# Kernel optimization log

Hardware: AMD Instinct MI355X
Metric: run time of the kernel (lower is better)

## Reference

```python
import jax, jax.numpy as jnp
import numpy as np

EPS = 1e-6
NUM_HEADS = 16


def _layernorm(x, g, b):
    m = jnp.mean(x, axis=-1, keepdims=True)
    v = jnp.mean(jnp.square(x - m), axis=-1, keepdims=True)
    return (x - m) * jax.lax.rsqrt(v + EPS) * g + b


def setup_inputs() -> dict:
    key = jax.random.key(0)
    ks = jax.random.split(key, 16)
    B, Lq, Lkv, D = 2, 2048, 4096, 2048
    Hd = D // NUM_HEADS
    s = 0.02
    return {
        "hidden_states": jax.random.normal(ks[0], (B, Lq, D), jnp.float32),
        "cross_attention_states": jax.random.normal(ks[1], (B, Lkv, D), jnp.float32),
        "q_w": jax.random.normal(ks[2], (D, D), jnp.float32) * s,
        "q_b": jnp.zeros((D,), jnp.float32),
        "k_w": jax.random.normal(ks[3], (D, D), jnp.float32) * s,
        "k_b": jnp.zeros((D,), jnp.float32),
        "v_w": jax.random.normal(ks[4], (D, D), jnp.float32) * s,
        "v_b": jnp.zeros((D,), jnp.float32),
        "o_w": jax.random.normal(ks[5], (D, D), jnp.float32) * s,
        "o_b": jnp.zeros((D,), jnp.float32),
        "qn_g": jnp.ones((Hd,), jnp.float32),
        "qn_b": jnp.zeros((Hd,), jnp.float32),
        "kn_g": jnp.ones((Hd,), jnp.float32),
        "kn_b": jnp.zeros((Hd,), jnp.float32),
    }


def reference(hidden_states, cross_attention_states,
              q_w, q_b, k_w, k_b, v_w, v_b, o_w, o_b,
              qn_g, qn_b, kn_g, kn_b):
    B, Lq, D = hidden_states.shape
    H = NUM_HEADS
    Hd = D // H
    scale = Hd ** -0.5

    # torch Linear: y = x @ W^T + b
    q = hidden_states @ q_w.T + q_b                        # [B,Lq,D]
    k = cross_attention_states @ k_w.T + k_b               # [B,Lkv,D]
    v = cross_attention_states @ v_w.T + v_b               # [B,Lkv,D]

    q = q.reshape(B, Lq, H, Hd).transpose(0, 2, 1, 3)      # [B,H,Lq,Hd]
    k = k.reshape(B, -1, H, Hd).transpose(0, 2, 1, 3)      # [B,H,Lkv,Hd]
    v = v.reshape(B, -1, H, Hd).transpose(0, 2, 1, 3)      # [B,H,Lkv,Hd]

    # per-head QK LayerNorm before scores
    q = _layernorm(q, qn_g, qn_b)
    k = _layernorm(k, kn_g, kn_b)

    attn_weights = jnp.einsum('bhqd,bhkd->bhqk', q, k) * scale
    attn_weights = jax.nn.softmax(attn_weights.astype(jnp.float32), axis=-1).astype(q.dtype)
    # dropout p=0.0 (inference) -> identity

    attn_output = jnp.einsum('bhqk,bhkd->bhqd', attn_weights, v)
    attn_output = attn_output.transpose(0, 2, 1, 3).reshape(B, Lq, D)
    attn_output = attn_output @ o_w.T + o_b
    return attn_output, attn_weights
```

## Files before the change

### kernel.cpp

```cpp
#include <hip/hip_runtime.h>
#include <cstdint>
#include <cstddef>

using u16 = unsigned short;
using f32x4 = __attribute__((ext_vector_type(4))) float;
using bf8   = __attribute__((ext_vector_type(8))) short;
using u32x4 = __attribute__((ext_vector_type(4))) unsigned;

#define DEVFN __device__ __forceinline__

constexpr int BB  = 2;
constexpr int LQ  = 2048;
constexpr int LKV = 4096;
constexpr int DD  = 2048;
constexpr int NH  = 16;
constexpr int HDm = 128;
constexpr float ATTN_SCALE = 0.08838834764831845f;
constexpr float LN_EPS = 1e-6f;
constexpr float LOG2E  = 1.4426950408889634f;
constexpr float SHIFT2 = 17.312340490667562f;

DEVFN u16 f2bf(float f) {
  unsigned u = __builtin_bit_cast(unsigned, f);
  u += 0x7fffu + ((u >> 16) & 1u);
  return (u16)(u >> 16);
}
DEVFN float bf2f(u16 h) { return __builtin_bit_cast(float, (unsigned)h << 16); }
DEVFN f32x4 mfma16(bf8 a, bf8 b, f32x4 c) {
  return __builtin_amdgcn_mfma_f32_16x16x32_bf16(a, b, c, 0, 0, 0);
}
DEVFN void gl16(const void* g, void* l) {
  __builtin_amdgcn_global_load_lds(
      (const __attribute__((address_space(1))) void*)g,
      (__attribute__((address_space(3))) void*)l, 16, 0, 0);
}
DEVFN void barrier_hard() {
  __builtin_amdgcn_s_barrier();
  __builtin_amdgcn_sched_barrier(0);
}

__global__ __launch_bounds__(256) void k_cvt(const float4* __restrict__ in,
                                             ushort4* __restrict__ out, int n4) {
  int i = blockIdx.x * 256 + threadIdx.x;
  if (i >= n4) return;
  float4 v = in[i];
  ushort4 o;
  o.x = f2bf(v.x); o.y = f2bf(v.y); o.z = f2bf(v.z); o.w = f2bf(v.w);
  out[i] = o;
}

template <int MODE>
__global__ __launch_bounds__(256) void k_gemm_nt(const u16* __restrict__ X,
                                                 const u16* __restrict__ Wt,
                                                 const float* __restrict__ bias,
                                                 const float* __restrict__ lng,
                                                 const float* __restrict__ lnb,
                                                 void* __restrict__ Y,
                                                 int M, int N, int K) {
  __shared__ __align__(16) u16 Sh[2][128 * 64];
  __shared__ float Sm[2][128], Sq[2][128];
  u16* As = Sh[0];
  u16* Bs = Sh[1];
  const int tid = threadIdx.x;
  const int w = tid >> 6, l = tid & 63;
  const int m0 = blockIdx.x * 128, n0 = blockIdx.y * 128;
  const int wr = w >> 1, wc = w & 1;
  const int lr = l & 15, lk = (l >> 4) * 8;
  const int rsw = (l & 7) << 3;
  const int srow = l >> 3;
  const int scb = (l & 7) * 16;
  f32x4 acc[4][4] = {};

  for (int k0 = 0; k0 < K; k0 += 64) {
#pragma unroll
    for (int i = 0; i < 4; ++i) {
      int rbase = w * 32 + i * 8;
      int row = rbase + srow;
      int cb = scb ^ ((row & 7) << 4);
      gl16((const char*)&X[(size_t)(m0 + row) * K + k0] + cb, &As[rbase * 64]);
      gl16((const char*)&Wt[(size_t)(n0 + row) * K + k0] + cb, &Bs[rbase * 64]);
    }
    __syncthreads();
    bf8 af[4][2], bfr[4][2];
#pragma unroll
    for (int mi = 0; mi < 4; ++mi)
#pragma unroll
      for (int kk = 0; kk < 2; ++kk)
        af[mi][kk] = *(const bf8*)&As[(wr * 64 + mi * 16 + lr) * 64 + ((kk * 32 + lk) ^ rsw)];
#pragma unroll
    for (int ni = 0; ni < 4; ++ni)
#pragma unroll
      for (int kk = 0; kk < 2; ++kk)
        bfr[ni][kk] = *(const bf8*)&Bs[(wc * 64 + ni * 16 + lr) * 64 + ((kk * 32 + lk) ^ rsw)];
#pragma unroll
    for (int kk = 0; kk < 2; ++kk)
#pragma unroll
      for (int mi = 0; mi < 4; ++mi)
#pragma unroll
        for (int ni = 0; ni < 4; ++ni)
          acc[mi][ni] = mfma16(af[mi][kk], bfr[ni][kk], acc[mi][ni]);
    __syncthreads();
  }
  const int lrg = (l >> 4) * 4;

  float bv[4];
#pragma unroll
  for (int ni = 0; ni < 4; ++ni) bv[ni] = bias[n0 + wc * 64 + ni * 16 + lr];
#pragma unroll
  for (int mi = 0; mi < 4; ++mi)
#pragma unroll
    for (int ni = 0; ni < 4; ++ni)
#pragma unroll
      for (int r = 0; r < 4; ++r) acc[mi][ni][r] += bv[ni];

  if constexpr (MODE == 2 || MODE == 3) {
#pragma unroll
    for (int mi = 0; mi < 4; ++mi) {
#pragma unroll
      for (int r = 0; r < 4; ++r) {
        float ps = 0.f, pq = 0.f;
#pragma unroll
        for (int ni = 0; ni < 4; ++ni) {
          float v = acc[mi][ni][r];
          ps += v; pq += v * v;
        }
#pragma unroll
        for (int m = 1; m < 16; m <<= 1) {
          ps += __shfl_xor(ps, m);
          pq += __shfl_xor(pq, m);
        }
        if (lr == 0) {
          int rl = wr * 64 + mi * 16 + lrg + r;
          Sm[wc][rl] = ps; Sq[wc][rl] = pq;
        }
      }
    }
    __syncthreads();
    float gv[4], bbv[4];
#pragma unroll
    for (int ni = 0; ni < 4; ++ni) {
      int c = wc * 64 + ni * 16 + lr;
      gv[ni] = lng[c]; bbv[ni] = lnb[c];
    }
#pragma unroll
    for (int mi = 0; mi < 4; ++mi)
#pragma unroll
      for (int r = 0; r < 4; ++r) {
        int rl = wr * 64 + mi * 16 + lrg + r;
        float mean = (Sm[0][rl] + Sm[1][rl]) * (1.f / 128.f);
        float var  = (Sq[0][rl] + Sq[1][rl]) * (1.f / 128.f) - mean * mean;
        float rs = rsqrtf(var + LN_EPS);
#pragma unroll
        for (int ni = 0; ni < 4; ++ni) {
          float o = (acc[mi][ni][r] - mean) * rs * gv[ni] + bbv[ni];
          if (MODE == 3) o *= ATTN_SCALE;
          acc[mi][ni][r] = o;
        }
      }
  }

  if constexpr (MODE == 4) {
    u16* T = &Sh[0][0];
#pragma unroll
    for (int mi = 0; mi < 4; ++mi)
#pragma unroll
      for (int ni = 0; ni < 4; ++ni)
#pragma unroll
        for (int r = 0; r < 4; ++r) {
          int mrow = wr * 64 + mi * 16 + lrg + r;
          int ncol = wc * 64 + ni * 16 + lr;
          T[mrow * 128 + (ncol ^ ((mrow & 7) << 3))] = f2bf(acc[mi][ni][r]);
        }
    __syncthreads();
    int hd = tid >> 1, half = tid & 1;
    int bq = m0 >> 12;
    int kvb = (m0 & (LKV - 1)) + half * 64;
    int hh = n0 >> 7;
    u16* vout = (u16*)Y + ((size_t)(bq * NH + hh) * HDm + hd) * LKV + kvb;
#pragma unroll
    for (int j8 = 0; j8 < 8; ++j8) {
      u16 tmp[8] __attribute__((aligned(16)));
#pragma unroll
      for (int j = 0; j < 8; ++j) {
        int kv = half * 64 + j8 * 8 + j;
        tmp[j] = T[kv * 128 + (hd ^ ((kv & 7) << 3))];
      }
      *(int4*)&vout[j8 * 8] = *(const int4*)tmp;
    }
    return;
  }

#pragma unroll
  for (int ni = 0; ni < 4; ++ni) {
    int n = n0 + wc * 64 + ni * 16 + lr;
#pragma unroll
    for (int mi = 0; mi < 4; ++mi) {
      int mb = m0 + wr * 64 + mi * 16 + lrg;
#pragma unroll
      for (int r = 0; r < 4; ++r) {
        float v = acc[mi][ni][r];
        if constexpr (MODE == 1)
          __builtin_nontemporal_store(v, &((float*)Y)[(size_t)(mb + r) * N + n]);
        else
          ((u16*)Y)[(size_t)(mb + r) * N + n] = f2bf(v);
      }
    }
  }
}

__global__ __launch_bounds__(256) void k_attn(const u16* __restrict__ Qp,
                                              const u16* __restrict__ Kp,
                                              const u16* __restrict__ Vt,
                                              float* __restrict__ Wout,
                                              u16* __restrict__ AO) {
  const int g = blockIdx.x;
  const int work = (g & 7) * 64 + (g >> 3);
  const int bh = work >> 4;
  const int b = bh >> 4, h = bh & 15;
  const int q0 = (work & 15) * 128;
  const int tid = threadIdx.x, w = tid >> 6, l = tid & 63;
  const int lr = l & 15, lk = (l >> 4) * 8;
  const int gq = l >> 4;
  const int rsw = (l & 7) << 3;
  __shared__ __align__(16) u16 Ks[2][64 * 128];
  __shared__ __align__(16) u16 Vs[2][128 * 64];

  bf8 qf[2][4];
#pragma unroll
  for (int qc = 0; qc < 2; ++qc) {
    const u16* qb = &Qp[((size_t)b * LQ + q0 + w * 32 + qc * 16 + lr) * DD + h * HDm];
#pragma unroll
    for (int kc = 0; kc < 4; ++kc) qf[qc][kc] = *(const bf8*)(qb + kc * 32 + lk);
  }
  const u16* Kb = Kp + (size_t)b * LKV * DD + h * HDm;
  const u16* Vb = Vt + (size_t)bh * HDm * LKV;

  auto stageK = [&](int buf, int kv0) {
#pragma unroll
    for (int i = 0; i < 4; ++i) {
      int rbase = w * 16 + i * 4;
      int row = rbase + (l >> 4);
      int cb = ((l & 15) * 16) ^ ((row & 7) << 4);
      gl16((const char*)(Kb + (size_t)(kv0 + row) * DD) + cb, &Ks[buf][rbase * 128]);
    }
  };
  auto stageV = [&](int buf, int kv0) {
#pragma unroll
    for (int i = 0; i < 4; ++i) {
      int rbase = w * 32 + i * 8;
      int row = rbase + (l >> 3);
      int cb = ((l & 7) * 16) ^ ((row & 7) << 4);
      gl16((const char*)(Vb + (size_t)row * LKV + kv0) + cb, &Vs[buf][rbase * 64]);
    }
  };
  auto stageK128 = [&](u16* buf, int kv0) {
#pragma unroll
    for (int i = 0; i < 8; ++i) {
      int rbase = w * 32 + i * 4;
      int row = rbase + (l >> 4);
      int cb = ((l & 15) * 16) ^ ((row & 7) << 4);
      gl16((const char*)(Kb + (size_t)(kv0 + row) * DD) + cb, &buf[rbase * 128]);
    }
  };

  u16* bufA0 = &Ks[0][0];
  u16* bufA1 = &Vs[0][0];
  float lsum[2] = {0.f, 0.f};
  stageK128(bufA0, 0);
  asm volatile("s_waitcnt vmcnt(0)" ::: "memory");
  barrier_hard();
  for (int t = 0; t < 32; ++t) {
    const u16* kb = (t & 1) ? bufA1 : bufA0;
    if (t < 31) stageK128((t & 1) ? bufA0 : bufA1, (t + 1) * 128);
#pragma unroll
    for (int ni = 0; ni < 8; ++ni) {
      f32x4 s0 = {0.f, 0.f, 0.f, 0.f}, s1 = {0.f, 0.f, 0.f, 0.f};
      __builtin_amdgcn_s_setprio(1);
#pragma unroll
      for (int kc = 0; kc < 4; ++kc) {
        bf8 kf = *(const bf8*)&kb[(ni * 16 + lr) * 128 + ((kc * 32 + lk) ^ rsw)];
        s0 = mfma16(kf, qf[0][kc], s0);
        s1 = mfma16(kf, qf[1][kc], s1);
      }
      __builtin_amdgcn_s_setprio(0);
#pragma unroll
      for (int r = 0; r < 4; ++r) {
        lsum[0] += exp2f(fmaf(s0[r], LOG2E, -SHIFT2));
        lsum[1] += exp2f(fmaf(s1[r], LOG2E, -SHIFT2));
      }
    }
    asm volatile("s_waitcnt vmcnt(0)" ::: "memory");
    barrier_hard();
  }
  float cr[2];
#pragma unroll
  for (int qc = 0; qc < 2; ++qc) {
    float v = lsum[qc];
    v += __shfl_xor(v, 16);
    v += __shfl_xor(v, 32);
    cr[qc] = -(SHIFT2 + __log2f(v));
  }

  f32x4 oacc[2][8] = {};
  float* wq0 = Wout + ((size_t)bh * LQ + q0 + w * 32 + lr) * LKV;
  float* wq1 = wq0 + (size_t)16 * LKV;
  const int srcA = lr + ((gq & 1) << 5);
  const int srcB = srcA + 16;
  const bool hi = (gq >> 1) != 0;

  stageK(0, 0); stageV(0, 0);
  asm volatile("s_waitcnt vmcnt(0)" ::: "memory");
  barrier_hard();
  for (int t = 0; t < 64; ++t) {
    const int cur = t & 1;
    const int kv0 = t * 64;
    if (t < 63) { stageK(cur ^ 1, kv0 + 64); stageV(cur ^ 1, kv0 + 64); }
    f32x4 s[2][4];
    __builtin_amdgcn_s_setprio(1);
#pragma unroll
    for (int ni = 0; ni < 4; ++ni) {
      s[0][ni] = f32x4{0.f, 0.f, 0.f, 0.f};
      s[1][ni] = f32x4{0.f, 0.f, 0.f, 0.f};
#pragma unroll
      for (int kc = 0; kc < 4; ++kc) {
        bf8 kf = *(const bf8*)&Ks[cur][(ni * 16 + lr) * 128 + ((kc * 32 + lk) ^ rsw)];
        s[0][ni] = mfma16(kf, qf[0][kc], s[0][ni]);
        s[1][ni] = mfma16(kf, qf[1][kc], s[1][ni]);
      }
    }
    __builtin_amdgcn_s_setprio(0);
    unsigned pk2[2][4][2];
#pragma unroll
    for (int qc = 0; qc < 2; ++qc) {
      float* wq = qc ? wq1 : wq0;
#pragma unroll
      for (int ni = 0; ni < 4; ++ni) {
        float p0 = exp2f(fmaf(s[qc][ni][0], LOG2E, cr[qc]));
        float p1 = exp2f(fmaf(s[qc][ni][1], LOG2E, cr[qc]));
        float p2 = exp2f(fmaf(s[qc][ni][2], LOG2E, cr[qc]));
        float p3 = exp2f(fmaf(s[qc][ni][3], LOG2E, cr[qc]));
        f32x4 pv4 = {p0, p1, p2, p3};
        __builtin_nontemporal_store(pv4, (f32x4*)(wq + kv0 + ni * 16 + 4 * gq));
        pk2[qc][ni][0] = (unsigned)f2bf(p0) | ((unsigned)f2bf(p1) << 16);
        pk2[qc][ni][1] = (unsigned)f2bf(p2) | ((unsigned)f2bf(p3) << 16);
      }
    }
#pragma unroll
    for (int kk = 0; kk < 2; ++kk) {
      bf8 pfq[2];
#pragma unroll
      for (int qc = 0; qc < 2; ++qc) {
        unsigned xa0 = __shfl(pk2[qc][2 * kk][0], srcA), xa1 = __shfl(pk2[qc][2 * kk][1], srcA);
        unsigned ya0 = __shfl(pk2[qc][2 * kk + 1][0], srcA), ya1 = __shfl(pk2[qc][2 * kk + 1][1], srcA);
        unsigned xb0 = __shfl(pk2[qc][2 * kk][0], srcB), xb1 = __shfl(pk2[qc][2 * kk][1], srcB);
        unsigned yb0 = __shfl(pk2[qc][2 * kk + 1][0], srcB), yb1 = __shfl(pk2[qc][2 * kk + 1][1], srcB);
        u32x4 pf32 = { hi ? ya0 : xa0, hi ? ya1 : xa1, hi ? yb0 : xb0, hi ? yb1 : xb1 };
        pfq[qc] = __builtin_bit_cast(bf8, pf32);
      }
      __builtin_amdgcn_s_setprio(1);
#pragma unroll
      for (int c = 0; c < 8; ++c) {
        bf8 vf = *(const bf8*)&Vs[cur][(c * 16 + lr) * 64 + ((kk * 32 + lk) ^ rsw)];
        oacc[0][c] = mfma16(pfq[0], vf, oacc[0][c]);
        oacc[1][c] = mfma16(pfq[1], vf, oacc[1][c]);
      }
      __builtin_amdgcn_s_setprio(0);
    }
    asm volatile("s_waitcnt vmcnt(8)" ::: "memory");
    barrier_hard();
  }

#pragma unroll
  for (int qc = 0; qc < 2; ++qc)
#pragma unroll
    for (int c = 0; c < 8; ++c)
#pragma unroll
      for (int r = 0; r < 4; ++r)
        AO[((size_t)b * LQ + q0 + w * 32 + qc * 16 + 4 * gq + r) * DD + h * HDm + c * 16 + lr] =
            f2bf(oacc[qc][c][r]);
}

extern "C" void kernel_launch(void* const* d_in, const int* in_sizes, int n_in,
                              void* d_out, int out_size, void* d_ws, size_t ws_size,
                              hipStream_t stream) {
  const float* hs   = (const float*)d_in[0];
  const float* cas  = (const float*)d_in[1];
  const float* q_w  = (const float*)d_in[2];
  const float* q_b  = (const float*)d_in[3];
  const float* k_w  = (const float*)d_in[4];
  const float* k_b  = (const float*)d_in[5];
  const float* v_w  = (const float*)d_in[6];
  const float* v_b  = (const float*)d_in[7];
  const float* o_w  = (const float*)d_in[8];
  const float* o_b  = (const float*)d_in[9];
  const float* qn_g = (const float*)d_in[10];
  const float* qn_b = (const float*)d_in[11];
  const float* kn_g = (const float*)d_in[12];
  const float* kn_b = (const float*)d_in[13];

  float* out_attn = (float*)d_out;
  float* out_w    = out_attn + (size_t)BB * LQ * DD;

  constexpr size_t SZ_Q  = (size_t)BB * LQ * DD * 2;
  constexpr size_t SZ_KV = (size_t)BB * LKV * DD * 2;
  constexpr size_t SZ_W  = (size_t)DD * DD * 2;
  char* p = (char*)d_ws;
  u16* hsb  = (u16*)p;              p += SZ_Q;
  u16* casb = (u16*)p;              p += SZ_KV;
  u16* qwb  = (u16*)p;              p += SZ_W;
  u16* kwb  = (u16*)p;              p += SZ_W;
  u16* vwb  = (u16*)p;              p += SZ_W;
  u16* owb  = (u16*)p;              p += SZ_W;
  u16* Qp   = (u16*)p;              p += SZ_Q;
  u16* Kp   = (u16*)p;              p += SZ_KV;
  u16* Vtp  = (u16*)p;              p += SZ_KV;
  u16* AO   = (u16*)p;              p += SZ_Q;

  auto cvt = [&](const float* src, u16* dst, size_t n) {
    int n4 = (int)(n / 4);
    k_cvt<<<dim3((n4 + 255) / 256), dim3(256), 0, stream>>>(
        (const float4*)src, (ushort4*)dst, n4);
  };
  cvt(hs,  hsb,  (size_t)BB * LQ * DD);
  cvt(cas, casb, (size_t)BB * LKV * DD);
  cvt(q_w, qwb, (size_t)DD * DD);
  cvt(k_w, kwb, (size_t)DD * DD);
  cvt(v_w, vwb, (size_t)DD * DD);
  cvt(o_w, owb, (size_t)DD * DD);

  k_gemm_nt<3><<<dim3(BB * LQ / 128, DD / 128), dim3(256), 0, stream>>>(
      hsb, qwb, q_b, qn_g, qn_b, Qp, BB * LQ, DD, DD);
  k_gemm_nt<2><<<dim3(BB * LKV / 128, DD / 128), dim3(256), 0, stream>>>(
      casb, kwb, k_b, kn_g, kn_b, Kp, BB * LKV, DD, DD);
  k_gemm_nt<4><<<dim3(BB * LKV / 128, DD / 128), dim3(256), 0, stream>>>(
      casb, vwb, v_b, nullptr, nullptr, Vtp, BB * LKV, DD, DD);

  k_attn<<<dim3(LQ / 128 * BB * NH), dim3(256), 0, stream>>>(Qp, Kp, Vtp, out_w, AO);

  k_gemm_nt<1><<<dim3(BB * LQ / 128, DD / 128), dim3(256), 0, stream>>>(
      AO, owb, o_b, nullptr, nullptr, out_attn, BB * LQ, DD, DD);
}
```

Baseline: 760.1 us.

## Double-buffer GEMM LDS tiles with 256x128 tiles and 512-thread blocks

```diff
diff --git a/kernel.cpp b/kernel.cpp
--- a/kernel.cpp
+++ b/kernel.cpp
@@ -50,20 +50,19 @@
 }
 
 template <int MODE>
-__global__ __launch_bounds__(256) void k_gemm_nt(const u16* __restrict__ X,
+__global__ __launch_bounds__(512) void k_gemm_nt(const u16* __restrict__ X,
                                                  const u16* __restrict__ Wt,
                                                  const float* __restrict__ bias,
                                                  const float* __restrict__ lng,
                                                  const float* __restrict__ lnb,
                                                  void* __restrict__ Y,
                                                  int M, int N, int K) {
-  __shared__ __align__(16) u16 Sh[2][128 * 64];
-  __shared__ float Sm[2][128], Sq[2][128];
-  u16* As = Sh[0];
-  u16* Bs = Sh[1];
+  __shared__ __align__(16) u16 As_[2][256 * 64];
+  __shared__ __align__(16) u16 Bs_[2][128 * 64];
+  __shared__ float Sm[2][256], Sq[2][256];
   const int tid = threadIdx.x;
   const int w = tid >> 6, l = tid & 63;
-  const int m0 = blockIdx.x * 128, n0 = blockIdx.y * 128;
+  const int m0 = blockIdx.x * 256, n0 = blockIdx.y * 128;
   const int wr = w >> 1, wc = w & 1;
   const int lr = l & 15, lk = (l >> 4) * 8;
   const int rsw = (l & 7) << 3;
@@ -71,35 +70,73 @@
   const int scb = (l & 7) * 16;
   f32x4 acc[4][4] = {};
 
-  for (int k0 = 0; k0 < K; k0 += 64) {
+  auto stage = [&](int buf, int k0) {
 #pragma unroll
     for (int i = 0; i < 4; ++i) {
-      int rbase = w * 32 + i * 8;
+      int rbase = i * 64 + w * 8;
       int row = rbase + srow;
       int cb = scb ^ ((row & 7) << 4);
-      gl16((const char*)&X[(size_t)(m0 + row) * K + k0] + cb, &As[rbase * 64]);
-      gl16((const char*)&Wt[(size_t)(n0 + row) * K + k0] + cb, &Bs[rbase * 64]);
-    }
-    __syncthreads();
-    bf8 af[4][2], bfr[4][2];
+      gl16((const char*)&X[(size_t)(m0 + row) * K + k0] + cb, &As_[buf][rbase * 64]);
+    }
+#pragma unroll
+    for (int i = 0; i < 2; ++i) {
+      int rbase = i * 64 + w * 8;
+      int row = rbase + srow;
+      int cb = scb ^ ((row & 7) << 4);
+      gl16((const char*)&Wt[(size_t)(n0 + row) * K + k0] + cb, &Bs_[buf][rbase * 64]);
+    }
+  };
+
+  const int NT = K >> 6;
+  stage(0, 0);
+  asm volatile("s_waitcnt vmcnt(0)" ::: "memory");
+  barrier_hard();
+  for (int kt = 0; kt < NT; ++kt) {
+    const int cur = kt & 1;
+    if (kt + 1 < NT) stage(cur ^ 1, (kt + 1) * 64);
+    bf8 af[4][2], bf01[2][2];
 #pragma unroll
     for (int mi = 0; mi < 4; ++mi)
 #pragma unroll
       for (int kk = 0; kk < 2; ++kk)
-        af[mi][kk] = *(const bf8*)&As[(wr * 64 + mi * 16 + lr) * 64 + ((kk * 32 + lk) ^ rsw)];
-#pragma unroll
-    for (int ni = 0; ni < 4; ++ni)
+        af[mi][kk] = *(const bf8*)&As_[cur][(wr * 64 + mi * 16 + lr) * 64 + ((kk * 32 + lk) ^ rsw)];
+#pragma unroll
+    for (int ni = 0; ni < 2; ++ni)
 #pragma unroll
       for (int kk = 0; kk < 2; ++kk)
-        bfr[ni][kk] = *(const bf8*)&Bs[(wc * 64 + ni * 16 + lr) * 64 + ((kk * 32 + lk) ^ rsw)];
+        bf01[ni][kk] = *(const bf8*)&Bs_[cur][(wc * 64 + ni * 16 + lr) * 64 + ((kk * 32 + lk) ^ rsw)];
+    __builtin_amdgcn_s_barrier();
+    asm volatile("s_waitcnt lgkmcnt(0)" ::: "memory");
+    __builtin_amdgcn_sched_barrier(0);
+    __builtin_amdgcn_s_setprio(1);
 #pragma unroll
     for (int kk = 0; kk < 2; ++kk)
 #pragma unroll
       for (int mi = 0; mi < 4; ++mi)
 #pragma unroll
-        for (int ni = 0; ni < 4; ++ni)
-          acc[mi][ni] = mfma16(af[mi][kk], bfr[ni][kk], acc[mi][ni]);
-    __syncthreads();
+        for (int ni = 0; ni < 2; ++ni)
+          acc[mi][ni] = mfma16(af[mi][kk], bf01[ni][kk], acc[mi][ni]);
+    __builtin_amdgcn_s_setprio(0);
+    __builtin_amdgcn_s_barrier();
+    bf8 bf23[2][2];
+#pragma unroll
+    for (int ni = 0; ni < 2; ++ni)
+#pragma unroll
+      for (int kk = 0; kk < 2; ++kk)
+        bf23[ni][kk] = *(const bf8*)&Bs_[cur][(wc * 64 + (ni + 2) * 16 + lr) * 64 + ((kk * 32 + lk) ^ rsw)];
+    asm volatile("s_waitcnt lgkmcnt(0)" ::: "memory");
+    __builtin_amdgcn_sched_barrier(0);
+    __builtin_amdgcn_s_setprio(1);
+#pragma unroll
+    for (int kk = 0; kk < 2; ++kk)
+#pragma unroll
+      for (int mi = 0; mi < 4; ++mi)
+#pragma unroll
+        for (int ni = 0; ni < 2; ++ni)
+          acc[mi][ni + 2] = mfma16(af[mi][kk], bf23[ni][kk], acc[mi][ni + 2]);
+    __builtin_amdgcn_s_setprio(0);
+    asm volatile("s_waitcnt vmcnt(0)" ::: "memory");
+    barrier_hard();
   }
   const int lrg = (l >> 4) * 4;
 
@@ -160,7 +197,8 @@
   }
 
   if constexpr (MODE == 4) {
-    u16* T = &Sh[0][0];
+    u16* T = &As_[0][0];
+    __syncthreads();
 #pragma unroll
     for (int mi = 0; mi < 4; ++mi)
 #pragma unroll
@@ -172,9 +210,9 @@
           T[mrow * 128 + (ncol ^ ((mrow & 7) << 3))] = f2bf(acc[mi][ni][r]);
         }
     __syncthreads();
-    int hd = tid >> 1, half = tid & 1;
+    int hd = tid >> 2, q4 = tid & 3;
     int bq = m0 >> 12;
-    int kvb = (m0 & (LKV - 1)) + half * 64;
+    int kvb = (m0 & (LKV - 1)) + q4 * 64;
     int hh = n0 >> 7;
     u16* vout = (u16*)Y + ((size_t)(bq * NH + hh) * HDm + hd) * LKV + kvb;
 #pragma unroll
@@ -182,7 +220,7 @@
       u16 tmp[8] __attribute__((aligned(16)));
 #pragma unroll
       for (int j = 0; j < 8; ++j) {
-        int kv = half * 64 + j8 * 8 + j;
+        int kv = q4 * 64 + j8 * 8 + j;
         tmp[j] = T[kv * 128 + (hd ^ ((kv & 7) << 3))];
       }
       *(int4*)&vout[j8 * 8] = *(const int4*)tmp;
@@ -428,15 +466,15 @@
   cvt(v_w, vwb, (size_t)DD * DD);
   cvt(o_w, owb, (size_t)DD * DD);
 
-  k_gemm_nt<3><<<dim3(BB * LQ / 128, DD / 128), dim3(256), 0, stream>>>(
+  k_gemm_nt<3><<<dim3(BB * LQ / 256, DD / 128), dim3(512), 0, stream>>>(
       hsb, qwb, q_b, qn_g, qn_b, Qp, BB * LQ, DD, DD);
-  k_gemm_nt<2><<<dim3(BB * LKV / 128, DD / 128), dim3(256), 0, stream>>>(
+  k_gemm_nt<2><<<dim3(BB * LKV / 256, DD / 128), dim3(512), 0, stream>>>(
       casb, kwb, k_b, kn_g, kn_b, Kp, BB * LKV, DD, DD);
-  k_gemm_nt<4><<<dim3(BB * LKV / 128, DD / 128), dim3(256), 0, stream>>>(
+  k_gemm_nt<4><<<dim3(BB * LKV / 256, DD / 128), dim3(512), 0, stream>>>(
       casb, vwb, v_b, nullptr, nullptr, Vtp, BB * LKV, DD, DD);
 
   k_attn<<<dim3(LQ / 128 * BB * NH), dim3(256), 0, stream>>>(Qp, Kp, Vtp, out_w, AO);
 
-  k_gemm_nt<1><<<dim3(BB * LQ / 128, DD / 128), dim3(256), 0, stream>>>(
+  k_gemm_nt<1><<<dim3(BB * LQ / 256, DD / 128), dim3(512), 0, stream>>>(
       AO, owb, o_b, nullptr, nullptr, out_attn, BB * LQ, DD, DD);
 }
```

Measured after the change: 798.5 us. 5.0% more time.
